# Kernel tuning notes

Measured on AMD Instinct MI355X. Metric: run time of the kernel, lower is better.

The kernel has to match this reference:

```python
import jax, jax.numpy as jnp
import numpy as np

N_NODES = 50000
N_EDGES = 800000
NFEAT, NHID, NCLASS = 512, 256, 64


def _glorot(key, fan_in, fan_out):
    # mimics kipf-style uniform init: U(-1/sqrt(fan_out), 1/sqrt(fan_out))
    stdv = 1.0 / np.sqrt(fan_out)
    return jax.random.uniform(key, (fan_in, fan_out), jnp.float32, -stdv, stdv)


def setup_inputs() -> dict:
    key = jax.random.key(0)
    ks = jax.random.split(key, 8)
    x = jax.random.normal(ks[0], (N_NODES, NFEAT), jnp.float32)
    edge_src = jax.random.randint(ks[1], (N_EDGES,), 0, N_NODES, jnp.int32)
    edge_dst = jax.random.randint(ks[2], (N_EDGES,), 0, N_NODES, jnp.int32)
    edge_weight = jax.random.uniform(ks[3], (N_EDGES,), jnp.float32)
    W1 = _glorot(ks[4], NFEAT, NHID)
    b1 = jax.random.uniform(ks[5], (NHID,), jnp.float32, -1.0 / np.sqrt(NHID), 1.0 / np.sqrt(NHID))
    W2 = _glorot(ks[6], NHID, NCLASS)
    b2 = jax.random.uniform(ks[7], (NCLASS,), jnp.float32, -1.0 / np.sqrt(NCLASS), 1.0 / np.sqrt(NCLASS))
    return {"x": x, "W1": W1, "b1": b1, "W2": W2, "b2": b2,
            "edge_weight": edge_weight, "edge_src": edge_src, "edge_dst": edge_dst}


def _spmm(edge_src, edge_dst, edge_weight, support):
    # adj @ support with adj given as COO edge list: out[d] += w * support[s]
    msgs = support[edge_src] * edge_weight[:, None]  # [E, F]
    return jax.ops.segment_sum(msgs, edge_dst, num_segments=N_NODES)


def reference(x, W1, b1, W2, b2, edge_weight, edge_src, edge_dst):
    # layer 1: GraphConvolution -> ReLU (dropout identity in eval mode)
    h = _spmm(edge_src, edge_dst, edge_weight, x @ W1) + b1
    h = jax.nn.relu(h)
    # layer 2: GraphConvolution -> log_softmax over classes
    logits = _spmm(edge_src, edge_dst, edge_weight, h @ W2) + b2
    return jax.nn.log_softmax(logits, axis=1)
```

## Files before the change

kernel.cpp:

```cpp
#include <hip/hip_runtime.h>
#include <cstdint>


typedef unsigned char u8;
typedef unsigned short u16;
typedef unsigned int u32;
typedef unsigned long long u64;
typedef __attribute__((ext_vector_type(8))) short bf16x8;
typedef __attribute__((ext_vector_type(4))) float f32x4;
typedef __attribute__((ext_vector_type(2))) float f32x2;

#define N_NODES 50000
#define N_EDGES 800000
#define NFEAT 512
#define NHID 256
#define NCLASS 64
#define CSTRIDE 64

#define NBUCK 196
#define BCAP 5120
#define SCB 391
#define GB1 782
#define PW1B 512
#define PW2B 64
#define FNB 3125

__device__ __forceinline__ float bf2f(u16 h) {
    union { u32 u; float f; } c; c.u = ((u32)h) << 16; return c.f;
}
__device__ __forceinline__ u16 f2bf(float f) {
    union { float f; u32 u; } c; c.f = f;
    u32 u = c.u;
    return (u16)((u + 0x7fffu + ((u >> 16) & 1u)) >> 16);
}
__device__ __forceinline__ u32 pk2(float a, float b) {
    return (u32)f2bf(a) | ((u32)f2bf(b) << 16);
}
__device__ __forceinline__ u8 f2f8(float f) {
    f = fmaxf(fminf(f, 448.f), -448.f);
    return (u8)(__builtin_amdgcn_cvt_pk_fp8_f32(f, f, 0, false) & 0xFF);
}

__device__ __forceinline__ void async16(const void* g, void* l) {
    __builtin_amdgcn_global_load_lds(
        (const __attribute__((address_space(1))) void*)(uintptr_t)g,
        (__attribute__((address_space(3))) void*)(uintptr_t)l, 16, 0, 0);
}


__global__ __launch_bounds__(256) void prep_scatter_kernel(
    const float* __restrict__ W1, u16* __restrict__ W1T,
    const float* __restrict__ W2, u16* __restrict__ W2T,
    const int* __restrict__ esrc, const int* __restrict__ edst,
    const float* __restrict__ ew, int* __restrict__ fill, u64* __restrict__ region) {
    __shared__ int cnt[NBUCK];
    __shared__ int base[NBUCK];
    int b = blockIdx.x, tid = threadIdx.x;
    if (b < SCB) {
        if (tid < NBUCK) cnt[tid] = 0;
        __syncthreads();
        int e0 = b * 2048 + tid * 8;
        int d[8], s[8], rk[8];
        float w[8];
        bool act = (e0 < N_EDGES);
        if (act) {
            int4 d0 = *(const int4*)(edst + e0),  d1 = *(const int4*)(edst + e0 + 4);
            int4 s0 = *(const int4*)(esrc + e0),  s1 = *(const int4*)(esrc + e0 + 4);
            float4 w0 = *(const float4*)(ew + e0), w1 = *(const float4*)(ew + e0 + 4);
            d[0]=d0.x; d[1]=d0.y; d[2]=d0.z; d[3]=d0.w;
            d[4]=d1.x; d[5]=d1.y; d[6]=d1.z; d[7]=d1.w;
            s[0]=s0.x; s[1]=s0.y; s[2]=s0.z; s[3]=s0.w;
            s[4]=s1.x; s[5]=s1.y; s[6]=s1.z; s[7]=s1.w;
            w[0]=w0.x; w[1]=w0.y; w[2]=w0.z; w[3]=w0.w;
            w[4]=w1.x; w[5]=w1.y; w[6]=w1.z; w[7]=w1.w;
            #pragma unroll
            for (int i = 0; i < 8; ++i)
                rk[i] = atomicAdd(&cnt[d[i] >> 8], 1);
        }
        __syncthreads();
        if (tid < NBUCK) base[tid] = atomicAdd(&fill[tid], cnt[tid]);
        __syncthreads();
        if (act) {
            #pragma unroll
            for (int i = 0; i < 8; ++i) {
                int g = d[i] >> 8;
                int pos = base[g] + rk[i];
                if (pos < BCAP) {
                    u64 en = ((u64)(d[i] & 255) << 32) |
                             (u64)((u32)s[i] | ((u32)f2bf(w[i]) << 16));
                    region[(size_t)g * BCAP + pos] = en;
                }
            }
        }
    } else if (b < SCB + PW1B) {
        int idx = (b - SCB) * 256 + tid;
        int n = idx >> 9, k = idx & 511;
        W1T[idx] = f2bf(W1[(size_t)k * NHID + n]);
    } else {
        int idx = (b - SCB - PW1B) * 256 + tid;
        int n = idx >> 8, k = idx & 255;
        W2T[idx] = f2bf(W2[(size_t)k * NCLASS + n]);
    }
}


__device__ __forceinline__ void gemm1_body(const float* __restrict__ x,
                                           const u16* __restrict__ BT,
                                           u8* __restrict__ C, int M,
                                           int bid, u16* lds) {
    u16* As = lds;
    u16* Bs = lds + 64 * 64;

    const int tid  = threadIdx.x;
    const int wv   = tid >> 6, lane = tid & 63;
    const int lm   = lane & 15, quad = lane >> 4;
    const int wcol = wv;
    const int m0   = bid * 64;
    const int co0 = ((0 * 4 + quad) ^ (lm & 7)) * 8;
    const int co1 = ((1 * 4 + quad) ^ (lm & 7)) * 8;

    f32x4 acc[4][4];
    #pragma unroll
    for (int r = 0; r < 4; ++r)
        #pragma unroll
        for (int c = 0; c < 4; ++c) acc[r][c] = (f32x4){0.f, 0.f, 0.f, 0.f};

    for (int k0 = 0; k0 < NFEAT; k0 += 64) {
        int row = tid >> 2, ko = (tid & 3) * 16;
        int gr = m0 + row; if (gr > M - 1) gr = M - 1;
        const float4* gp = (const float4*)(x + (size_t)gr * NFEAT + k0 + ko);
        float4 f0 = gp[0], f1 = gp[1], f2 = gp[2], f3 = gp[3];
        #pragma unroll
        for (int i = 0; i < 8; ++i) {
            int c = i * 256 + tid;
            int n = c >> 3, kb = c & 7;
            async16(BT + (size_t)n * NFEAT + k0 + ((kb ^ (n & 7)) * 8), Bs + c * 8);
        }
        u32 p[8] = {pk2(f0.x, f0.y), pk2(f0.z, f0.w), pk2(f1.x, f1.y), pk2(f1.z, f1.w),
                    pk2(f2.x, f2.y), pk2(f2.z, f2.w), pk2(f3.x, f3.y), pk2(f3.z, f3.w)};
        int ch0 = (2 * (tid & 3))     ^ (row & 7);
        int ch1 = (2 * (tid & 3) + 1) ^ (row & 7);
        *(int4*)(As + row * 64 + ch0 * 8) = *(int4*)&p[0];
        *(int4*)(As + row * 64 + ch1 * 8) = *(int4*)&p[4];
        __syncthreads();

        #pragma unroll
        for (int kk = 0; kk < 2; ++kk) {
            const int co = kk ? co1 : co0;
            bf16x8 af[4], bfv[4];
            #pragma unroll
            for (int rt = 0; rt < 4; ++rt)
                af[rt] = *(const bf16x8*)(As + (rt * 16 + lm) * 64 + co);
            #pragma unroll
            for (int ct = 0; ct < 4; ++ct) {
                int n = wcol * 64 + ct * 16 + lm;
                bfv[ct] = *(const bf16x8*)(Bs + n * 64 + co);
            }
            #pragma unroll
            for (int rt = 0; rt < 4; ++rt)
                #pragma unroll
                for (int ct = 0; ct < 4; ++ct)
                    acc[rt][ct] = __builtin_amdgcn_mfma_f32_16x16x32_bf16(
                        af[rt], bfv[ct], acc[rt][ct], 0, 0, 0);
        }
        __syncthreads();
    }

    u8* lds8 = (u8*)lds;
    #pragma unroll
    for (int rt = 0; rt < 4; ++rt)
        #pragma unroll
        for (int ct = 0; ct < 4; ++ct) {
            int col = wcol * 64 + ct * 16 + lm;
            #pragma unroll
            for (int r = 0; r < 4; ++r) {
                int row = rt * 16 + quad * 4 + r;
                lds8[row * 256 + col] = f2f8(acc[rt][ct][r]);
            }
        }
    __syncthreads();
    #pragma unroll
    for (int i = 0; i < 4; ++i) {
        int c = i * 256 + tid;
        int row = c >> 4, ch = c & 15;
        if (m0 + row < M)
            *(int4*)(C + (size_t)(m0 + row) * 256 + ch * 16) = *(const int4*)(lds8 + c * 16);
    }
}


__global__ __launch_bounds__(256) void gemm1_sort_kernel(
    const float* __restrict__ x, const u16* __restrict__ W1T, u8* __restrict__ S8,
    const u64* __restrict__ region, const int* __restrict__ fill,
    u32* __restrict__ csr, int* __restrict__ deg) {
    __shared__ __align__(16) u16 lds[(64 + 256) * 64];
    int b = blockIdx.x, tid = threadIdx.x;
    if (b < NBUCK) {
        int* cnt2 = (int*)lds;
        cnt2[tid] = 0;
        __syncthreads();
        int Eb = fill[b]; if (Eb > BCAP) Eb = BCAP;
        for (int i = tid; i < Eb; i += 256) {
            u64 en = region[(size_t)b * BCAP + i];
            int dlo = (int)(en >> 32) & 255;
            int r = atomicAdd(&cnt2[dlo], 1);
            if (r < CSTRIDE)
                csr[(size_t)(b * 256 + dlo) * CSTRIDE + r] = (u32)en;
        }
        __syncthreads();
        int node = b * 256 + tid;
        if (node < N_NODES) {
            int dg = cnt2[tid]; if (dg > CSTRIDE) dg = CSTRIDE;
            deg[node] = dg;
        }
    } else {
        gemm1_body(x, W1T, S8, N_NODES, b - NBUCK, lds);
    }
}


__global__ __launch_bounds__(256) void spmm1_gemm2_kernel(
    const u8* __restrict__ S8, const int* __restrict__ deg,
    const u32* __restrict__ csr, const float* __restrict__ bias1,
    const u16* __restrict__ W2T, u16* __restrict__ S2) {
    __shared__ __align__(16) u16 Hs[16 * 256];

    const int tid  = threadIdx.x;
    const int wv   = tid >> 6, lane = tid & 63;
    const int lm   = lane & 15, quad = lane >> 4;
    const int b    = blockIdx.x;

    float4 bv = *(const float4*)(bias1 + lane * 4);

    int begs[4], degs[4];
    int maxd = 0;
    #pragma unroll
    for (int n = 0; n < 4; ++n) {
        int node = __builtin_amdgcn_readfirstlane(b * 16 + wv * 4 + n);
        begs[n] = node * CSTRIDE;
        degs[n] = deg[node];
        maxd = max(maxd, degs[n]);
    }

    float a[4][4];
    #pragma unroll
    for (int n = 0; n < 4; ++n)
        #pragma unroll
        for (int k = 0; k < 4; ++k) a[n][k] = 0.f;

    for (int kb = 0; kb < maxd; kb += 8) {
        u32 e[4][8];
        #pragma unroll
        for (int n = 0; n < 4; ++n)
            #pragma unroll
            for (int i = 0; i < 8; ++i) {
                u32 t = csr[begs[n] + kb + i];
                e[n][i] = (kb + i < degs[n]) ? t : 0u;
            }
        u32 q[4][8];
        #pragma unroll
        for (int n = 0; n < 4; ++n)
            #pragma unroll
            for (int i = 0; i < 8; ++i)
                q[n][i] = *(const u32*)(S8 + (size_t)(e[n][i] & 0xFFFFu) * NHID + lane * 4);
        #pragma unroll
        for (int n = 0; n < 4; ++n)
            #pragma unroll
            for (int i = 0; i < 8; ++i) {
                float w = bf2f((u16)(e[n][i] >> 16));
                f32x2 lo = __builtin_amdgcn_cvt_pk_f32_fp8((int)q[n][i], false);
                f32x2 hi = __builtin_amdgcn_cvt_pk_f32_fp8((int)q[n][i], true);
                a[n][0] += w * lo.x; a[n][1] += w * lo.y;
                a[n][2] += w * hi.x; a[n][3] += w * hi.y;
            }
    }

    #pragma unroll
    for (int n = 0; n < 4; ++n) {
        int lrow = wv * 4 + n;
        float a0 = fmaxf(a[n][0] + bv.x, 0.f);
        float a1 = fmaxf(a[n][1] + bv.y, 0.f);
        float a2 = fmaxf(a[n][2] + bv.z, 0.f);
        float a3 = fmaxf(a[n][3] + bv.w, 0.f);
        int ch = (lane >> 1) ^ (lrow & 7);
        u32* dp = (u32*)(Hs + lrow * 256 + ch * 8 + (lane & 1) * 4);
        dp[0] = pk2(a0, a1);
        dp[1] = pk2(a2, a3);
    }
    __syncthreads();

    f32x4 acc = (f32x4){0.f, 0.f, 0.f, 0.f};
    #pragma unroll
    for (int k0 = 0; k0 < NHID; k0 += 64) {
        #pragma unroll
        for (int kk = 0; kk < 2; ++kk) {
            int ca = ((k0 >> 3) + kk * 4 + quad) ^ (lm & 7);
            bf16x8 af = *(const bf16x8*)(Hs + lm * 256 + ca * 8);
            int n = wv * 16 + lm;
            bf16x8 bf = *(const bf16x8*)(W2T + (size_t)n * NHID + k0 + kk * 32 + quad * 8);
            acc = __builtin_amdgcn_mfma_f32_16x16x32_bf16(af, bf, acc, 0, 0, 0);
        }
    }
    __syncthreads();

    #pragma unroll
    for (int r = 0; r < 4; ++r) {
        int row = quad * 4 + r;
        Hs[row * 64 + wv * 16 + lm] = f2bf(acc[r]);
    }
    __syncthreads();
    *(ushort4*)(S2 + (size_t)b * 1024 + tid * 4) = *(const ushort4*)(Hs + tid * 4);
}


__global__ __launch_bounds__(256) void spmm_bias_lsm_kernel(
    const u16* __restrict__ S, const int* __restrict__ deg,
    const u32* __restrict__ csr, const float* __restrict__ bias,
    float* __restrict__ out) {
    const int tid = threadIdx.x;
    const int wv = tid >> 6, lane = tid & 63;
    const int b = blockIdx.x;

    int begs[4], degs[4];
    int maxd = 0;
    #pragma unroll
    for (int n = 0; n < 4; ++n) {
        int node = __builtin_amdgcn_readfirstlane(b * 16 + wv * 4 + n);
        begs[n] = node * CSTRIDE;
        degs[n] = deg[node];
        maxd = max(maxd, degs[n]);
    }

    float acc[4] = {0.f, 0.f, 0.f, 0.f};
    for (int kb = 0; kb < maxd; kb += 8) {
        u32 e[4][8];
        #pragma unroll
        for (int n = 0; n < 4; ++n)
            #pragma unroll
            for (int i = 0; i < 8; ++i) {
                u32 t = csr[begs[n] + kb + i];
                e[n][i] = (kb + i < degs[n]) ? t : 0u;
            }
        u16 v[4][8];
        #pragma unroll
        for (int n = 0; n < 4; ++n)
            #pragma unroll
            for (int i = 0; i < 8; ++i)
                v[n][i] = S[(size_t)(e[n][i] & 0xFFFFu) * NCLASS + lane];
        #pragma unroll
        for (int n = 0; n < 4; ++n)
            #pragma unroll
            for (int i = 0; i < 8; ++i)
                acc[n] += bf2f((u16)(e[n][i] >> 16)) * bf2f(v[n][i]);
    }

    float bl = bias[lane];
    #pragma unroll
    for (int n = 0; n < 4; ++n) {
        int node = b * 16 + wv * 4 + n;
        float x = acc[n] + bl;
        float m = x;
        #pragma unroll
        for (int off = 32; off > 0; off >>= 1) m = fmaxf(m, __shfl_xor(m, off));
        float e = expf(x - m);
        float ssum = e;
        #pragma unroll
        for (int off = 32; off > 0; off >>= 1) ssum += __shfl_xor(ssum, off);
        out[(size_t)node * NCLASS + lane] = x - m - logf(ssum);
    }
}


extern "C" void kernel_launch(void* const* d_in, const int* in_sizes, int n_in,
                              void* d_out, int out_size, void* d_ws, size_t ws_size,
                              hipStream_t stream) {
    const float* x  = (const float*)d_in[0];
    const float* W1 = (const float*)d_in[1];
    const float* b1 = (const float*)d_in[2];
    const float* W2 = (const float*)d_in[3];
    const float* b2 = (const float*)d_in[4];
    const float* ew = (const float*)d_in[5];
    const int* esrc = (const int*)d_in[6];
    const int* edst = (const int*)d_in[7];
    float* out = (float*)d_out;

    char* ws = (char*)d_ws;
    size_t off = 0;
    auto take = [&](size_t bytes) -> void* {
        off = (off + 255) & ~(size_t)255;
        void* p = ws + off;
        off += bytes;
        return p;
    };
    u8*  S8   = (u8*)take((size_t)N_NODES * NHID);
    u16* S2   = (u16*)take((size_t)N_NODES * NCLASS * 2);
    u16* W1T  = (u16*)take((size_t)NHID * NFEAT * 2);
    u16* W2T  = (u16*)take((size_t)NCLASS * NHID * 2);
    int* deg  = (int*)take((size_t)N_NODES * 4);
    u32* csr  = (u32*)take((size_t)N_NODES * CSTRIDE * 4);
    int* fill = (int*)take((size_t)NBUCK * 4);
    u64* region = (u64*)take((size_t)NBUCK * BCAP * 8);
    (void)ws_size; (void)in_sizes; (void)n_in; (void)out_size;

    hipMemsetAsync(fill, 0, (size_t)NBUCK * 4, stream);
    prep_scatter_kernel<<<SCB + PW1B + PW2B, 256, 0, stream>>>(
        W1, W1T, W2, W2T, esrc, edst, ew, fill, region);
    gemm1_sort_kernel<<<NBUCK + GB1, 256, 0, stream>>>(
        x, W1T, S8, region, fill, csr, deg);
    spmm1_gemm2_kernel<<<FNB, 256, 0, stream>>>(S8, deg, csr, b1, W2T, S2);
    spmm_bias_lsm_kernel<<<FNB, 256, 0, stream>>>(S2, deg, csr, b2, out);
}
```

Measured before the change: 259.9 us.

## Software-pipeline GEMM1 K-loop with double-buffered A tile and prefetched x loads

Restructures the GEMM1 K-loop so the next x tile's global loads are issued before the MFMA compute of the current tile. A is double-buffered in LDS, and B's async copy for the next k-step is issued right after compute. Explicit s_waitcnt, s_barrier and sched_barrier replace __syncthreads to control ordering. The goal is to hide global load latency behind MFMA work, at the cost of more LDS, more live registers, and fragile manual synchronisation.

```diff
diff --git a/kernel.cpp b/kernel.cpp
--- a/kernel.cpp
+++ b/kernel.cpp
@@ -108,8 +108,8 @@
                                            const u16* __restrict__ BT,
                                            u8* __restrict__ C, int M,
                                            int bid, u16* lds) {
-    u16* As = lds;
-    u16* Bs = lds + 64 * 64;
+    u16* As0 = lds;
+    u16* Bs  = lds + 2 * 4096;
 
     const int tid  = threadIdx.x;
     const int wv   = tid >> 6, lane = tid & 63;
@@ -118,6 +118,11 @@
     const int m0   = bid * 64;
     const int co0 = ((0 * 4 + quad) ^ (lm & 7)) * 8;
     const int co1 = ((1 * 4 + quad) ^ (lm & 7)) * 8;
+    const int arow = tid >> 2;
+    int gr = m0 + arow; if (gr > M - 1) gr = M - 1;
+    const float* gpb = x + (size_t)gr * NFEAT + (tid & 3) * 16;
+    const int ch0 = (2 * (tid & 3)) ^ (arow & 7);
+    const int ch1 = (2 * (tid & 3) + 1) ^ (arow & 7);
 
     f32x4 acc[4][4];
     #pragma unroll
@@ -125,24 +130,32 @@
         #pragma unroll
         for (int c = 0; c < 4; ++c) acc[r][c] = (f32x4){0.f, 0.f, 0.f, 0.f};
 
-    for (int k0 = 0; k0 < NFEAT; k0 += 64) {
-        int row = tid >> 2, ko = (tid & 3) * 16;
-        int gr = m0 + row; if (gr > M - 1) gr = M - 1;
-        const float4* gp = (const float4*)(x + (size_t)gr * NFEAT + k0 + ko);
-        float4 f0 = gp[0], f1 = gp[1], f2 = gp[2], f3 = gp[3];
-        #pragma unroll
-        for (int i = 0; i < 8; ++i) {
-            int c = i * 256 + tid;
-            int n = c >> 3, kb = c & 7;
-            async16(BT + (size_t)n * NFEAT + k0 + ((kb ^ (n & 7)) * 8), Bs + c * 8);
-        }
+    float4 f0, f1, f2, f3;
+    {
+        const float4* gp = (const float4*)gpb;
+        f0 = gp[0]; f1 = gp[1]; f2 = gp[2]; f3 = gp[3];
+    }
+    #pragma unroll
+    for (int i = 0; i < 8; ++i) {
+        int c = i * 256 + tid;
+        int n = c >> 3, kb = c & 7;
+        async16(BT + (size_t)n * NFEAT + ((kb ^ (n & 7)) * 8), Bs + c * 8);
+    }
+
+    for (int t = 0; t < 8; ++t) {
+        u16* As = As0 + (t & 1) * 4096;
         u32 p[8] = {pk2(f0.x, f0.y), pk2(f0.z, f0.w), pk2(f1.x, f1.y), pk2(f1.z, f1.w),
                     pk2(f2.x, f2.y), pk2(f2.z, f2.w), pk2(f3.x, f3.y), pk2(f3.z, f3.w)};
-        int ch0 = (2 * (tid & 3))     ^ (row & 7);
-        int ch1 = (2 * (tid & 3) + 1) ^ (row & 7);
-        *(int4*)(As + row * 64 + ch0 * 8) = *(int4*)&p[0];
-        *(int4*)(As + row * 64 + ch1 * 8) = *(int4*)&p[4];
-        __syncthreads();
+        *(int4*)(As + arow * 64 + ch0 * 8) = *(int4*)&p[0];
+        *(int4*)(As + arow * 64 + ch1 * 8) = *(int4*)&p[4];
+        asm volatile("s_waitcnt vmcnt(0) lgkmcnt(0)" ::: "memory");
+        __builtin_amdgcn_sched_barrier(0);
+        if (t < 7) {
+            const float4* gp = (const float4*)(gpb + (t + 1) * 64);
+            f0 = gp[0]; f1 = gp[1]; f2 = gp[2]; f3 = gp[3];
+        }
+        __builtin_amdgcn_s_barrier();
+        __builtin_amdgcn_sched_barrier(0);
 
         #pragma unroll
         for (int kk = 0; kk < 2; ++kk) {
@@ -163,7 +176,17 @@
                     acc[rt][ct] = __builtin_amdgcn_mfma_f32_16x16x32_bf16(
                         af[rt], bfv[ct], acc[rt][ct], 0, 0, 0);
         }
-        __syncthreads();
+        __builtin_amdgcn_s_barrier();
+        __builtin_amdgcn_sched_barrier(0);
+        if (t < 7) {
+            int k0 = (t + 1) * 64;
+            #pragma unroll
+            for (int i = 0; i < 8; ++i) {
+                int c = i * 256 + tid;
+                int n = c >> 3, kb = c & 7;
+                async16(BT + (size_t)n * NFEAT + k0 + ((kb ^ (n & 7)) * 8), Bs + c * 8);
+            }
+        }
     }
 
     u8* lds8 = (u8*)lds;
@@ -193,7 +216,7 @@
     const float* __restrict__ x, const u16* __restrict__ W1T, u8* __restrict__ S8,
     const u64* __restrict__ region, const int* __restrict__ fill,
     u32* __restrict__ csr, int* __restrict__ deg) {
-    __shared__ __align__(16) u16 lds[(64 + 256) * 64];
+    __shared__ __align__(16) u16 lds[24576];
     int b = blockIdx.x, tid = threadIdx.x;
     if (b < NBUCK) {
         int* cnt2 = (int*)lds;
```

Result: no change. 256.1 us (-1.5%).
